# Performance work log

Measured on AMD Instinct MI355X. Metric: run time of the kernel, lower is better.

The kernel has to match this reference:

```python
import jax, jax.numpy as jnp
import numpy as np

N_NODES = 100000
HIDDEN = 64
REPR = 64
N_CHANNELS = 9
N_EDGES = 500000
NEG_SLOPE = 0.2


def _gat_layer(x, W, a_src, a_dst, b, src, dst, n_nodes):
    """PyG GATConv, heads=1, add_self_loops=True, eval mode (no dropout)."""
    # add self loops
    loop = jnp.arange(n_nodes, dtype=src.dtype)
    src = jnp.concatenate([src, loop])
    dst = jnp.concatenate([dst, loop])
    h = x @ W                                   # [N, F_out]
    s_src = h @ a_src                           # [N]
    s_dst = h @ a_dst                           # [N]
    e = s_src[src] + s_dst[dst]                 # [E+N]
    e = jnp.where(e > 0, e, NEG_SLOPE * e)      # leaky_relu
    # per-destination softmax (segment softmax)
    m = jax.ops.segment_max(e, dst, num_segments=n_nodes)
    m = jax.lax.stop_gradient(m)
    ex = jnp.exp(e - m[dst])
    denom = jax.ops.segment_sum(ex, dst, num_segments=n_nodes)
    alpha = ex / denom[dst]
    out = jax.ops.segment_sum(alpha[:, None] * h[src], dst, num_segments=n_nodes)
    return out + b


def setup_inputs() -> dict:
    key = jax.random.key(0)
    ks = jax.random.split(key, 12)
    g_h = 1.0 / np.sqrt(HIDDEN)
    g_r = 1.0 / np.sqrt(REPR)
    inp = {
        "embeddings": jax.random.normal(ks[0], (N_NODES, HIDDEN), jnp.float32) * g_h,
        "W1": jax.random.normal(ks[1], (N_CHANNELS, HIDDEN, HIDDEN), jnp.float32) * g_h,
        "a_src1": jax.random.normal(ks[2], (N_CHANNELS, HIDDEN), jnp.float32) * g_h,
        "a_dst1": jax.random.normal(ks[3], (N_CHANNELS, HIDDEN), jnp.float32) * g_h,
        "b1": jnp.zeros((N_CHANNELS, HIDDEN), jnp.float32),
        "W2": jax.random.normal(ks[4], (N_CHANNELS, HIDDEN, REPR), jnp.float32) * g_h,
        "a_src2": jax.random.normal(ks[5], (N_CHANNELS, REPR), jnp.float32) * g_r,
        "a_dst2": jax.random.normal(ks[6], (N_CHANNELS, REPR), jnp.float32) * g_r,
        "b2": jnp.zeros((N_CHANNELS, REPR), jnp.float32),
        "att": jax.random.normal(ks[7], (N_CHANNELS, REPR), jnp.float32) * g_r,
        "edge_indices": jax.random.randint(ks[8], (N_CHANNELS, 2, 2, N_EDGES), 0, N_NODES, jnp.int32),
    }
    return inp


def reference(embeddings, W1, a_src1, a_dst1, b1, W2, a_src2, a_dst2, b2, att, edge_indices):
    outs = []
    for c in range(N_CHANNELS):  # fixed small set of meta-path channels
        e0 = edge_indices[c, 0]
        e1 = edge_indices[c, 1]
        x1 = _gat_layer(embeddings, W1[c], a_src1[c], a_dst1[c], b1[c], e0[0], e0[1], N_NODES)
        x1 = jax.nn.relu(x1)
        x2 = _gat_layer(x1, W2[c], a_src2[c], a_dst2[c], b2[c], e1[0], e1[1], N_NODES)
        outs.append(x2)
    x = jnp.stack(outs, axis=1)                          # [N, C, repr]
    scores = jnp.einsum('ncd,cd->nc', x, att)            # [N, C]
    w = jax.nn.softmax(scores, axis=-1)                  # channel attention
    return jnp.einsum('ncd,nc->nd', x, w)                # [N, repr]
```

## Files before the change

kernel.cpp:

```cpp
#include <hip/hip_runtime.h>
#include <hip/hip_bf16.h>
#include <math.h>

#define N_NODES   100000
#define N_CH      9
#define N_EDG     500000
#define NEG_SLOPE 0.2f
#define NBINS     N_NODES
#define NSLOT     10
#define PACK_STRIDE 500016

#define CHUNK  4096
#define NBLK   123
#define NBUCK  391
#define MLEN   (NBUCK * NBLK)
#define NBA1   188
#define BCAP   4096


__device__ __forceinline__ float bf2f(unsigned short h) {
  return __uint_as_float(((unsigned)h) << 16);
}
__device__ __forceinline__ float bflo(unsigned u) { return __uint_as_float(u << 16); }
__device__ __forceinline__ float bfhi(unsigned u) { return __uint_as_float(u & 0xffff0000u); }
__device__ __forceinline__ unsigned short f2bf(float f) {
  unsigned u = __float_as_uint(f);
  u += 0x7FFFu + ((u >> 16) & 1u);
  return (unsigned short)(u >> 16);
}
__device__ __forceinline__ float lrelu(float x) { return x > 0.f ? x : NEG_SLOPE * x; }
__device__ __forceinline__ int clampi(int x) {
  return x < 0 ? 0 : (x >= N_NODES ? N_NODES - 1 : x);
}

__global__ __launch_bounds__(256) void write_const(float* __restrict__ out, float val) {
  int idx = blockIdx.x * 256 + threadIdx.x;
  out[idx] = val;
}

#define GEMM_BODY(LOAD_A)                                                     \
  __shared__ float Ws[64 * 64];                                               \
  __shared__ float Xs[64 * 132];                                              \
  __shared__ float redS[128 * 17];   \
  __shared__ float redD[128 * 17];                                            \
  const int tx = threadIdx.x;                                                 \
  const int r0 = blockIdx.x * 128;                                            \
  _Pragma("unroll")                                                           \
  for (int i = 0; i < 16; ++i) Ws[tx + 256 * i] = W[tx + 256 * i];            \
  _Pragma("unroll")                                                           \
  for (int it = 0; it < 8; ++it) {                                            \
    int f = tx + 256 * it;                                                    \
    int r = f >> 4;                                                           \
    int k0 = (f & 15) << 2;                                                   \
    float4 v = make_float4(0.f, 0.f, 0.f, 0.f);                               \
    if (r0 + r < M) { LOAD_A }                                                \
    Xs[(k0 + 0) * 132 + r] = v.x;                                             \
    Xs[(k0 + 1) * 132 + r] = v.y;                                             \
    Xs[(k0 + 2) * 132 + r] = v.z;                                             \
    Xs[(k0 + 3) * 132 + r] = v.w;                                             \
  }                                                                           \
  __syncthreads();                                                            \
  const int cg = tx & 15, rg = tx >> 4;                                       \
  float acc[8][4];                                                            \
  _Pragma("unroll")                                                           \
  for (int i = 0; i < 8; ++i)                                                 \
    _Pragma("unroll")                                                         \
    for (int j = 0; j < 4; ++j) acc[i][j] = 0.f;                              \
  _Pragma("unroll 4")                                                         \
  for (int k = 0; k < 64; ++k) {                                              \
    float4 w4 = *(const float4*)(Ws + k * 64 + cg * 4);                       \
    float4 x0 = *(const float4*)(Xs + k * 132 + rg * 8);                      \
    float4 x1 = *(const float4*)(Xs + k * 132 + rg * 8 + 4);                  \
    float xr[8] = {x0.x, x0.y, x0.z, x0.w, x1.x, x1.y, x1.z, x1.w};           \
    float wr[4] = {w4.x, w4.y, w4.z, w4.w};                                   \
    _Pragma("unroll")                                                         \
    for (int i = 0; i < 8; ++i)                                               \
      _Pragma("unroll")                                                       \
      for (int j = 0; j < 4; ++j) acc[i][j] += xr[i] * wr[j];                 \
  }                                                                           \
  float4 s4 = *(const float4*)(a_src + cg * 4);                               \
  float4 d4 = *(const float4*)(a_dst + cg * 4);                               \
  _Pragma("unroll")                                                           \
  for (int i = 0; i < 8; ++i) {                                               \
    int row = rg * 8 + i;                                                     \
    redS[row * 17 + cg] =                                                     \
        acc[i][0] * s4.x + acc[i][1] * s4.y + acc[i][2] * s4.z + acc[i][3] * s4.w; \
    redD[row * 17 + cg] =                                                     \
        acc[i][0] * d4.x + acc[i][1] * d4.y + acc[i][2] * d4.z + acc[i][3] * d4.w; \
    int r = r0 + row;                                                         \
    if (r < M) {                                                              \
      ushort4 o;                                                              \
      o.x = f2bf(acc[i][0]); o.y = f2bf(acc[i][1]);                           \
      o.z = f2bf(acc[i][2]); o.w = f2bf(acc[i][3]);                           \
      *(ushort4*)(Hout + (size_t)r * 64 + cg * 4) = o;                        \
    }                                                                         \
  }                                                                           \
  __syncthreads();                                                            \
  if (tx < 128) {                                                             \
    float s = 0.f;                                                            \
    _Pragma("unroll")                                                         \
    for (int c2 = 0; c2 < 16; ++c2) s += redS[tx * 17 + c2];                  \
    if (r0 + tx < M) sS[r0 + tx] = s;                                         \
  } else {                                                                    \
    int row = tx - 128;                                                       \
    float s = 0.f;                                                            \
    _Pragma("unroll")                                                         \
    for (int c2 = 0; c2 < 16; ++c2) s += redD[row * 17 + c2];                 \
    if (r0 + row < M) sD[r0 + row] = s;                                       \
  }

__global__ __launch_bounds__(256) void gemm64_f32(const float* __restrict__ A,
                                                  const float* __restrict__ W,
                                                  const float* __restrict__ a_src,
                                                  const float* __restrict__ a_dst,
                                                  unsigned short* __restrict__ Hout,
                                                  float* __restrict__ sS,
                                                  float* __restrict__ sD, int M) {
  GEMM_BODY(v = *(const float4*)(A + (size_t)(r0 + r) * 64 + k0);)
}

__global__ __launch_bounds__(256) void gemm64_bf(const unsigned short* __restrict__ A,
                                                 const float* __restrict__ W,
                                                 const float* __restrict__ a_src,
                                                 const float* __restrict__ a_dst,
                                                 unsigned short* __restrict__ Hout,
                                                 float* __restrict__ sS,
                                                 float* __restrict__ sD, int M) {
  GEMM_BODY(ushort4 h = *(const ushort4*)(A + (size_t)(r0 + r) * 64 + k0);
            v.x = bf2f(h.x); v.y = bf2f(h.y); v.z = bf2f(h.z); v.w = bf2f(h.w);)
}


__global__ __launch_bounds__(256) void histA(const int* __restrict__ EI, int base,
                                             int* __restrict__ histM) {
  const int g = blockIdx.y;
  const int* dst = EI + ((size_t)(base + g) * 2 + 1) * N_EDG;
  __shared__ int h[NBUCK];
  for (int i = threadIdx.x; i < NBUCK; i += 256) h[i] = 0;
  __syncthreads();
  const int e0 = blockIdx.x * CHUNK;
#pragma unroll
  for (int k = 0; k < CHUNK; k += 256) {
    int i = e0 + k + threadIdx.x;
    if (i < N_EDG) atomicAdd(&h[clampi(dst[i]) >> 8], 1);
  }
  __syncthreads();
  for (int i = threadIdx.x; i < NBUCK; i += 256)
    histM[(size_t)g * MLEN + i * NBLK + blockIdx.x] = h[i];
}

__global__ __launch_bounds__(256) void scanA1(int* __restrict__ data,
                                              int* __restrict__ bsum) {
  const int g = blockIdx.y;
  __shared__ int sh[256];
  int i = blockIdx.x * 256 + threadIdx.x;
  int x = (i < MLEN) ? data[(size_t)g * MLEN + i] : 0;
  sh[threadIdx.x] = x;
  __syncthreads();
  for (int off = 1; off < 256; off <<= 1) {
    int t = (threadIdx.x >= off) ? sh[threadIdx.x - off] : 0;
    __syncthreads();
    sh[threadIdx.x] += t;
    __syncthreads();
  }
  if (i < MLEN) data[(size_t)g * MLEN + i] = sh[threadIdx.x] - x;
  if (threadIdx.x == 255) bsum[g * 512 + blockIdx.x] = sh[255];
}

__global__ __launch_bounds__(512) void scanA2(int* __restrict__ bsum) {
  const int g = blockIdx.x;
  __shared__ int sh[512];
  int x = (threadIdx.x < NBA1) ? bsum[g * 512 + threadIdx.x] : 0;
  sh[threadIdx.x] = x;
  __syncthreads();
  for (int off = 1; off < 512; off <<= 1) {
    int t = (threadIdx.x >= off) ? sh[threadIdx.x - off] : 0;
    __syncthreads();
    sh[threadIdx.x] += t;
    __syncthreads();
  }
  if (threadIdx.x < NBA1) bsum[g * 512 + threadIdx.x] = sh[threadIdx.x] - x;
}

__global__ void scanA3(int* __restrict__ data, const int* __restrict__ bsum) {
  const int g = blockIdx.y;
  int i = blockIdx.x * 256 + threadIdx.x;
  if (i < MLEN) data[(size_t)g * MLEN + i] += bsum[g * 512 + blockIdx.x];
}

__global__ __launch_bounds__(256) void scatterA(const int* __restrict__ EI, int base,
                                                const int* __restrict__ histM,
                                                unsigned* __restrict__ pack) {
  const int g = blockIdx.y;
  const int* srcp = EI + ((size_t)(base + g) * 2 + 0) * N_EDG;
  const int* dstp = EI + ((size_t)(base + g) * 2 + 1) * N_EDG;
  __shared__ unsigned ed[CHUNK];
  __shared__ unsigned short bkt[CHUNK];
  __shared__ int lcnt[NBUCK];
  __shared__ int ebase[NBUCK];
  __shared__ int gbase[NBUCK];
  __shared__ int sc[512];
  const int t = threadIdx.x;
  const int e0 = blockIdx.x * CHUNK;
  const int nE = (N_EDG - e0 < CHUNK) ? (N_EDG - e0) : CHUNK;

  for (int i = t; i < NBUCK; i += 256) {
    lcnt[i] = 0;
    gbase[i] = histM[(size_t)g * MLEN + i * NBLK + blockIdx.x];
  }
  __syncthreads();
  for (int k = t; k < nE; k += 256)
    atomicAdd(&lcnt[clampi(dstp[e0 + k]) >> 8], 1);
  __syncthreads();
  int v0 = (t < NBUCK) ? lcnt[t] : 0;
  int v1 = (t + 256 < NBUCK) ? lcnt[t + 256] : 0;
  sc[t] = v0; sc[t + 256] = v1;
  __syncthreads();
  for (int off = 1; off < 512; off <<= 1) {
    int a0 = (t >= off) ? sc[t - off] : 0;
    int a1 = (t + 256 >= off) ? sc[t + 256 - off] : 0;
    __syncthreads();
    sc[t] += a0; sc[t + 256] += a1;
    __syncthreads();
  }
  if (t < NBUCK)       { ebase[t] = sc[t] - v0;             lcnt[t] = 0; }
  if (t + 256 < NBUCK) { ebase[t + 256] = sc[t + 256] - v1; lcnt[t + 256] = 0; }
  __syncthreads();
  for (int k = t; k < nE; k += 256) {
    int d = clampi(dstp[e0 + k]);
    int s = clampi(srcp[e0 + k]);
    int b = d >> 8;
    int slot = ebase[b] + atomicAdd(&lcnt[b], 1);
    ed[slot] = ((unsigned)s << 8) | (unsigned)(d & 255);
    bkt[slot] = (unsigned short)b;
  }
  __syncthreads();
  unsigned* pk = pack + (size_t)g * PACK_STRIDE;
  for (int i = t; i < nE; i += 256) {
    int b = bkt[i];
    pk[gbase[b] + (i - ebase[b])] = ed[i];
  }
}

__global__ __launch_bounds__(256) void sortB(const int* __restrict__ histM,
                                             unsigned* __restrict__ pack,
                                             int* __restrict__ rp) {
  const int g = blockIdx.y;
  const int b = blockIdx.x;
  __shared__ unsigned ed[BCAP];
  __shared__ unsigned ed2[BCAP];
  __shared__ int cnt[256];
  __shared__ int sh[256];
  const int t = threadIdx.x;
  const int beg = histM[(size_t)g * MLEN + b * NBLK];
  const int end = (b + 1 < NBUCK) ? histM[(size_t)g * MLEN + (b + 1) * NBLK] : N_EDG;
  int m = end - beg;
  if (m > BCAP) m = BCAP;
  unsigned* pk = pack + (size_t)g * PACK_STRIDE;

  cnt[t] = 0;
  __syncthreads();
  for (int i = t; i < m; i += 256) {
    unsigned w = pk[beg + i];
    ed[i] = w;
    atomicAdd(&cnt[w & 255u], 1);
  }
  __syncthreads();
  int x = cnt[t];
  sh[t] = x;
  __syncthreads();
  for (int off = 1; off < 256; off <<= 1) {
    int tt = (t >= off) ? sh[t - off] : 0;
    __syncthreads();
    sh[t] += tt;
    __syncthreads();
  }
  int n = b * 256 + t;
  if (n < N_NODES) rp[(size_t)g * NBINS + n] = beg + sh[t];
  cnt[t] = sh[t] - x;
  __syncthreads();
  for (int i = t; i < m; i += 256) {
    unsigned w = ed[i];
    int pos = atomicAdd(&cnt[w & 255u], 1);
    ed2[pos] = w >> 8;
  }
  __syncthreads();
  for (int i = t; i < m; i += 256) pk[beg + i] = ed2[i];
}

__global__ __launch_bounds__(256) void aggregate(const unsigned short* __restrict__ H,
                                                 const float* __restrict__ sS,
                                                 const float* __restrict__ sD,
                                                 const int* __restrict__ rp,
                                                 const unsigned* __restrict__ pack,
                                                 const float* __restrict__ bias,
                                                 unsigned short* __restrict__ X1out,
                                                 const float* __restrict__ att_c,
                                                 float* __restrict__ O,
                                                 float* __restrict__ Mn,
                                                 float* __restrict__ Sn,
                                                 float* __restrict__ outF,
                                                 int mode, int first, int last) {
  const int n = blockIdx.x * 16 + (threadIdx.x >> 4);
  const int f = threadIdx.x & 15;
  const int beg = (n == 0) ? 0 : rp[n - 1];
  const int end = rp[n];
  const float sDn = sD[n];
  const float wself = __expf(lrelu(sS[n] + sDn));

  uint2 hs = *(const uint2*)(H + ((size_t)n << 6) + (f << 2));
  float a0 = wself * bflo(hs.x);
  float a1 = wself * bfhi(hs.x);
  float a2 = wself * bflo(hs.y);
  float a3 = wself * bfhi(hs.y);
  float den = wself;

  uint2 h[4];
  float ss[4];
  int vm[4];
  int j = beg;
  if (j < end) {
#pragma unroll
    for (int u = 0; u < 4; ++u) {
      unsigned p = pack[j + u];
      vm[u] = (j + u < end);
      int s = vm[u] ? (int)p : n;
      h[u] = *(const uint2*)(H + ((size_t)s << 6) + (f << 2));
      ss[u] = sS[s];
    }
  }

  for (; j < end; j += 4) {
    const int jn = j + 4;
    uint2 hn[4] = {hs, hs, hs, hs};
    float ssn[4] = {0.f, 0.f, 0.f, 0.f};
    int vn[4] = {0, 0, 0, 0};
    if (jn < end) {
#pragma unroll
      for (int u = 0; u < 4; ++u) {
        unsigned p = pack[jn + u];
        vn[u] = (jn + u < end);
        int s = vn[u] ? (int)p : n;
        hn[u] = *(const uint2*)(H + ((size_t)s << 6) + (f << 2));
        ssn[u] = sS[s];
      }
    }
#pragma unroll
    for (int u = 0; u < 4; ++u) {
      float w = vm[u] ? __expf(lrelu(ss[u] + sDn)) : 0.f;
      den += w;
      a0 += w * bflo(h[u].x);
      a1 += w * bfhi(h[u].x);
      a2 += w * bflo(h[u].y);
      a3 += w * bfhi(h[u].y);
    }
#pragma unroll
    for (int u = 0; u < 4; ++u) { h[u] = hn[u]; ss[u] = ssn[u]; vm[u] = vn[u]; }
  }

  float v0 = a0 / den + bias[f * 4 + 0];
  float v1 = a1 / den + bias[f * 4 + 1];
  float v2 = a2 / den + bias[f * 4 + 2];
  float v3 = a3 / den + bias[f * 4 + 3];

  if (mode == 0) {
    ushort4 o;
    o.x = f2bf(v0 > 0.f ? v0 : 0.f);
    o.y = f2bf(v1 > 0.f ? v1 : 0.f);
    o.z = f2bf(v2 > 0.f ? v2 : 0.f);
    o.w = f2bf(v3 > 0.f ? v3 : 0.f);
    *(ushort4*)(X1out + (size_t)n * 64 + f * 4) = o;
  } else {
    float sc = v0 * att_c[f * 4 + 0] + v1 * att_c[f * 4 + 1] +
               v2 * att_c[f * 4 + 2] + v3 * att_c[f * 4 + 3];
    sc += __shfl_xor(sc, 1, 16);
    sc += __shfl_xor(sc, 2, 16);
    sc += __shfl_xor(sc, 4, 16);
    sc += __shfl_xor(sc, 8, 16);
    if (first) {
      *(float4*)(O + (size_t)n * 64 + f * 4) = make_float4(v0, v1, v2, v3);
      if (f == 0) { Mn[n] = sc; Sn[n] = 1.f; }
    } else {
      float M = Mn[n];
      float nM = fmaxf(M, sc);
      float scale = __expf(M - nM);
      float wch = __expf(sc - nM);
      float4 o4 = *(const float4*)(O + (size_t)n * 64 + f * 4);
      float o0 = o4.x * scale + wch * v0;
      float o1 = o4.y * scale + wch * v1;
      float o2 = o4.z * scale + wch * v2;
      float o3 = o4.w * scale + wch * v3;
      float s = Sn[n] * scale + wch;
      if (last) {
        *(float4*)(outF + (size_t)n * 64 + f * 4) =
            make_float4(o0 / s, o1 / s, o2 / s, o3 / s);
      } else {
        *(float4*)(O + (size_t)n * 64 + f * 4) = make_float4(o0, o1, o2, o3);
        if (f == 0) { Mn[n] = nM; Sn[n] = s; }
      }
    }
  }
}


extern "C" void kernel_launch(void* const* d_in, const int* in_sizes, int n_in,
                              void* d_out, int out_size, void* d_ws, size_t ws_size,
                              hipStream_t stream) {
  const float* emb = (const float*)d_in[0];
  const float* W1  = (const float*)d_in[1];
  const float* aS1 = (const float*)d_in[2];
  const float* aD1 = (const float*)d_in[3];
  const float* b1  = (const float*)d_in[4];
  const float* W2  = (const float*)d_in[5];
  const float* aS2 = (const float*)d_in[6];
  const float* aD2 = (const float*)d_in[7];
  const float* b2  = (const float*)d_in[8];
  const float* att = (const float*)d_in[9];
  const int*   EI  = (const int*)d_in[10];
  float* out = (float*)d_out;

  const int gElem = (N_NODES * 64) / 256;

  const size_t NEEDED = 53200000;
  if (ws_size < NEEDED) {
    write_const<<<gElem, 256, 0, stream>>>(out, 1000.0f + (float)(ws_size >> 20));
    return;
  }

  float* ws = (float*)d_ws;
  size_t off = 0;
  float* sS = ws + off; off += 100000;
  float* sD = ws + off; off += 100000;
  float* Mn = ws + off; off += 100000;
  float* Sn = ws + off; off += 100000;
  unsigned short* Hbf  = (unsigned short*)(ws + off); off += 3200000;
  unsigned short* X1bf = (unsigned short*)(ws + off); off += 3200000;
  int* histM     = (int*)(ws + off);      off += (size_t)NSLOT * MLEN + 64;
  int* bsumA     = (int*)(ws + off);      off += NSLOT * 512;
  int* rp        = (int*)(ws + off);      off += (size_t)NSLOT * NBINS;
  unsigned* pack = (unsigned*)(ws + off); off += (size_t)NSLOT * PACK_STRIDE;

  const int gGemm = (N_NODES + 127) / 128;
  const int gRow  = N_NODES / 16;

  auto build = [&](int base, int nG) {
    histA<<<dim3(NBLK, nG), 256, 0, stream>>>(EI, base, histM);
    scanA1<<<dim3(NBA1, nG), 256, 0, stream>>>(histM, bsumA);
    scanA2<<<nG, 512, 0, stream>>>(bsumA);
    scanA3<<<dim3(NBA1, nG), 256, 0, stream>>>(histM, bsumA);
    scatterA<<<dim3(NBLK, nG), 256, 0, stream>>>(EI, base, histM, pack);
    sortB<<<dim3(NBUCK, nG), 256, 0, stream>>>(histM, pack, rp);
  };

  build(0, 8);

  for (int c = 0; c < N_CH; ++c) {
    if (c == 4) build(8, 10);

    for (int layer = 0; layer < 2; ++layer) {
      const int gi = c * 2 + layer;
      const int slot = (gi < 8) ? gi : gi - 8;

      const float* Wf = (layer == 0) ? W1 + (size_t)c * 4096 : W2 + (size_t)c * 4096;
      const float* aS = (layer == 0) ? aS1 + c * 64 : aS2 + c * 64;
      const float* aD = (layer == 0) ? aD1 + c * 64 : aD2 + c * 64;
      const float* bb = (layer == 0) ? b1 + c * 64 : b2 + c * 64;

      if (layer == 0)
        gemm64_f32<<<gGemm, 256, 0, stream>>>(emb, Wf, aS, aD, Hbf, sS, sD, N_NODES);
      else
        gemm64_bf<<<gGemm, 256, 0, stream>>>(X1bf, Wf, aS, aD, Hbf, sS, sD, N_NODES);

      aggregate<<<gRow, 256, 0, stream>>>(Hbf, sS, sD,
                                          rp + (size_t)slot * NBINS,
                                          pack + (size_t)slot * PACK_STRIDE,
                                          bb, X1bf, att + c * 64,
                                          out, Mn, Sn, out,
                                          layer, (c == 0) ? 1 : 0, (c == N_CH - 1) ? 1 : 0);
    }
  }
}
```

Baseline: 1.084 ms.

## Reorder aggregate nodes by degree class to balance wavefront work

Adds a per-graph counting sort of destination nodes into degree classes (histogram, scan, scatter kernels) and has the aggregate kernel pick its node through the permutation. Nodes with similar in-degree then share a block, which is meant to cut divergence and idle lanes from uneven edge-loop lengths. In exchange there are three extra kernel launches per build and one extra indirection per node. The neighbouring nodes in a block are no longer contiguous, so loads of rp, H and sS/sD become scattered and outputs are written in permuted order.

```diff
diff --git a/kernel.cpp b/kernel.cpp
--- a/kernel.cpp
+++ b/kernel.cpp
@@ -16,6 +16,11 @@
 #define MLEN   (NBUCK * NBLK)
 #define NBA1   188
 #define BCAP   4096
+
+#define PCHUNK 4096
+#define NPBLK  25
+#define NCLS   16
+#define PMLEN  (NCLS * NPBLK)
 
 
 __device__ __forceinline__ float bf2f(unsigned short h) {
@@ -288,10 +293,95 @@
   for (int i = t; i < m; i += 256) pk[beg + i] = ed2[i];
 }
 
+
+__global__ __launch_bounds__(256) void histP(const int* __restrict__ rp,
+                                             int* __restrict__ histPM) {
+  const int g = blockIdx.y;
+  __shared__ int h[NCLS];
+  if (threadIdx.x < NCLS) h[threadIdx.x] = 0;
+  __syncthreads();
+  const int n0 = blockIdx.x * PCHUNK;
+  const int* rpg = rp + (size_t)g * NBINS;
+  for (int k = threadIdx.x; k < PCHUNK; k += 256) {
+    int n = n0 + k;
+    if (n < N_NODES) {
+      int deg = rpg[n] - (n ? rpg[n - 1] : 0);
+      int cls = (deg + 3) >> 2; if (cls > 15) cls = 15;
+      atomicAdd(&h[cls], 1);
+    }
+  }
+  __syncthreads();
+  if (threadIdx.x < NCLS)
+    histPM[(size_t)g * PMLEN + threadIdx.x * NPBLK + blockIdx.x] = h[threadIdx.x];
+}
+
+__global__ __launch_bounds__(512) void scanP(int* __restrict__ histPM) {
+  const int g = blockIdx.x;
+  __shared__ int sh[512];
+  int i = threadIdx.x;
+  int x = (i < PMLEN) ? histPM[(size_t)g * PMLEN + i] : 0;
+  sh[i] = x;
+  __syncthreads();
+  for (int off = 1; off < 512; off <<= 1) {
+    int t = (i >= off) ? sh[i - off] : 0;
+    __syncthreads();
+    sh[i] += t;
+    __syncthreads();
+  }
+  if (i < PMLEN) histPM[(size_t)g * PMLEN + i] = sh[i] - x;
+}
+
+__global__ __launch_bounds__(256) void scatterP(const int* __restrict__ rp,
+                                                const int* __restrict__ histPM,
+                                                int* __restrict__ perm) {
+  const int g = blockIdx.y;
+  __shared__ int ed[PCHUNK];
+  __shared__ unsigned char bkt[PCHUNK];
+  __shared__ int lcnt[NCLS], ebase[NCLS], gbase[NCLS], sc[NCLS];
+  const int t = threadIdx.x;
+  const int n0 = blockIdx.x * PCHUNK;
+  const int nN = (N_NODES - n0 < PCHUNK) ? (N_NODES - n0) : PCHUNK;
+  const int* rpg = rp + (size_t)g * NBINS;
+  if (t < NCLS) {
+    lcnt[t] = 0;
+    gbase[t] = histPM[(size_t)g * PMLEN + t * NPBLK + blockIdx.x];
+  }
+  __syncthreads();
+  for (int k = t; k < nN; k += 256) {
+    int n = n0 + k;
+    int deg = rpg[n] - (n ? rpg[n - 1] : 0);
+    int cls = (deg + 3) >> 2; if (cls > 15) cls = 15;
+    atomicAdd(&lcnt[cls], 1);
+  }
+  __syncthreads();
+  if (t == 0) {
+    int run = 0;
+    for (int c = 0; c < NCLS; ++c) { sc[c] = run; run += lcnt[c]; }
+  }
+  __syncthreads();
+  if (t < NCLS) { ebase[t] = sc[t]; lcnt[t] = 0; }
+  __syncthreads();
+  for (int k = t; k < nN; k += 256) {
+    int n = n0 + k;
+    int deg = rpg[n] - (n ? rpg[n - 1] : 0);
+    int cls = (deg + 3) >> 2; if (cls > 15) cls = 15;
+    int slot = ebase[cls] + atomicAdd(&lcnt[cls], 1);
+    ed[slot] = n;
+    bkt[slot] = (unsigned char)cls;
+  }
+  __syncthreads();
+  int* pm = perm + (size_t)g * NBINS;
+  for (int i = t; i < nN; i += 256) {
+    int c = bkt[i];
+    pm[gbase[c] + (i - ebase[c])] = ed[i];
+  }
+}
+
 __global__ __launch_bounds__(256) void aggregate(const unsigned short* __restrict__ H,
                                                  const float* __restrict__ sS,
                                                  const float* __restrict__ sD,
                                                  const int* __restrict__ rp,
+                                                 const int* __restrict__ perm,
                                                  const unsigned* __restrict__ pack,
                                                  const float* __restrict__ bias,
                                                  unsigned short* __restrict__ X1out,
@@ -301,7 +391,7 @@
                                                  float* __restrict__ Sn,
                                                  float* __restrict__ outF,
                                                  int mode, int first, int last) {
-  const int n = blockIdx.x * 16 + (threadIdx.x >> 4);
+  const int n = perm[blockIdx.x * 16 + (threadIdx.x >> 4)];
   const int f = threadIdx.x & 15;
   const int beg = (n == 0) ? 0 : rp[n - 1];
   const int end = rp[n];
@@ -421,7 +511,7 @@
 
   const int gElem = (N_NODES * 64) / 256;
 
-  const size_t NEEDED = 53200000;
+  const size_t NEEDED = 57500000;
   if (ws_size < NEEDED) {
     write_const<<<gElem, 256, 0, stream>>>(out, 1000.0f + (float)(ws_size >> 20));
     return;
@@ -438,6 +528,8 @@
   int* histM     = (int*)(ws + off);      off += (size_t)NSLOT * MLEN + 64;
   int* bsumA     = (int*)(ws + off);      off += NSLOT * 512;
   int* rp        = (int*)(ws + off);      off += (size_t)NSLOT * NBINS;
+  int* perm      = (int*)(ws + off);      off += (size_t)NSLOT * NBINS;
+  int* histPM    = (int*)(ws + off);      off += (size_t)NSLOT * PMLEN + 64;
   unsigned* pack = (unsigned*)(ws + off); off += (size_t)NSLOT * PACK_STRIDE;
 
   const int gGemm = (N_NODES + 127) / 128;
@@ -450,6 +542,9 @@
     scanA3<<<dim3(NBA1, nG), 256, 0, stream>>>(histM, bsumA);
     scatterA<<<dim3(NBLK, nG), 256, 0, stream>>>(EI, base, histM, pack);
     sortB<<<dim3(NBUCK, nG), 256, 0, stream>>>(histM, pack, rp);
+    histP<<<dim3(NPBLK, nG), 256, 0, stream>>>(rp, histPM);
+    scanP<<<nG, 512, 0, stream>>>(histPM);
+    scatterP<<<dim3(NPBLK, nG), 256, 0, stream>>>(rp, histPM, perm);
   };
 
   build(0, 8);
@@ -473,6 +568,7 @@
 
       aggregate<<<gRow, 256, 0, stream>>>(Hbf, sS, sD,
                                           rp + (size_t)slot * NBINS,
+                                          perm + (size_t)slot * NBINS,
                                           pack + (size_t)slot * PACK_STRIDE,
                                           bb, X1bf, att + c * 64,
                                           out, Mn, Sn, out,
```

Measured after the change: 1.116 ms. 1.03x slower.
